# Kernel optimization log

Measured on AMD Instinct MI355X. Metric: run time of the kernel, lower is better.

## Reference

```python
import jax, jax.numpy as jnp
import numpy as np

K = 3
STRIDE = 1
PAD = 1


def _conv(x, w, b):
    # NCHW conv, OIHW weight, stride/pad fixed
    y = jax.lax.conv_general_dilated(
        x, w, (STRIDE, STRIDE), [(PAD, PAD), (PAD, PAD)],
        dimension_numbers=("NCHW", "OIHW", "NCHW"))
    if b is not None:
        y = y + b[None, :, None, None]
    return y


def _deform_conv2d(x, offset, mask, weight):
    """torchvision.ops.deform_conv2d (modulated, groups=1, dilation=1, no bias)."""
    B, C, H, W = x.shape
    O = weight.shape[0]
    KK = K * K
    Ho, Wo = offset.shape[2], offset.shape[3]
    off = offset.reshape(B, KK, 2, Ho, Wo)
    off_y, off_x = off[:, :, 0], off[:, :, 1]
    ky = (jnp.arange(KK) // K).astype(x.dtype)  # kernel row offset
    kx = (jnp.arange(KK) % K).astype(x.dtype)   # kernel col offset
    base_y = (jnp.arange(Ho) * STRIDE - PAD).astype(x.dtype)
    base_x = (jnp.arange(Wo) * STRIDE - PAD).astype(x.dtype)
    # sampling positions [B, KK, Ho, Wo]
    py = base_y[None, None, :, None] + ky[None, :, None, None] + off_y
    px = base_x[None, None, None, :] + kx[None, :, None, None] + off_x

    y0 = jnp.floor(py)
    x0 = jnp.floor(px)
    wy = py - y0  # fractional parts
    wx = px - x0

    x_flat = x.reshape(B, C, H * W)

    def gather(yy, xx):
        valid = (yy >= 0) & (yy < H) & (xx >= 0) & (xx < W)
        yc = jnp.clip(yy, 0, H - 1).astype(jnp.int32)
        xc = jnp.clip(xx, 0, W - 1).astype(jnp.int32)
        idx = (yc * W + xc).reshape(B, -1)  # [B, KK*Ho*Wo]
        v = jax.vmap(lambda a, i: a[:, i])(x_flat, idx)  # [B, C, KK*Ho*Wo]
        v = v.reshape(B, C, KK, Ho, Wo)
        return v * valid.astype(x.dtype).reshape(B, 1, KK, Ho, Wo)

    samp = (gather(y0, x0) * ((1 - wy) * (1 - wx))[:, None]
            + gather(y0, x0 + 1) * ((1 - wy) * wx)[:, None]
            + gather(y0 + 1, x0) * (wy * (1 - wx))[:, None]
            + gather(y0 + 1, x0 + 1) * (wy * wx)[:, None])
    samp = samp * mask[:, None]  # modulation [B, C, KK, Ho, Wo]
    return jnp.einsum('bckhw,ock->bohw', samp, weight.reshape(O, C, KK))


def setup_inputs() -> dict:
    key = jax.random.key(0)
    ks = jax.random.split(key, 6)
    B, Cin, H, W, Cout = 4, 128, 128, 128, 256
    KK = K * K
    x = jax.random.normal(ks[0], (B, Cin, H, W), dtype=jnp.float32)
    # offset conv: trained weights are small (init at 0) -> scale down
    offset_w = 0.01 * jax.random.normal(ks[1], (2 * KK, Cin, K, K), dtype=jnp.float32)
    offset_b = 0.1 * jax.random.normal(ks[2], (2 * KK,), dtype=jnp.float32)
    mod_w = 0.1 * jax.random.normal(ks[3], (KK, Cin, K, K), dtype=jnp.float32)
    mod_b = 0.1 * jax.random.normal(ks[4], (KK,), dtype=jnp.float32)
    fan_in = Cin * KK
    weight = jax.random.normal(ks[5], (Cout, Cin, K, K), dtype=jnp.float32) / np.sqrt(fan_in)
    return {"x": x, "offset_w": offset_w, "offset_b": offset_b,
            "mod_w": mod_w, "mod_b": mod_b, "weight": weight}


def reference(x, offset_w, offset_b, mod_w, mod_b, weight):
    offset = _conv(x, offset_w, offset_b)
    modulator = 2.0 * jax.nn.sigmoid(_conv(x, mod_w, mod_b))
    return _deform_conv2d(x, offset, modulator, weight)
```

## Files before the change

kernel.cpp:

```cpp
#include <hip/hip_runtime.h>
#include <hip/hip_bf16.h>
#include <math.h>

#define CIN 128
#define HH 128
#define WW 128
#define HWX (HH*WW)
#define COUT 256
#define NB 4

typedef __attribute__((ext_vector_type(8))) short short8;
typedef __attribute__((ext_vector_type(4))) float f32x4;
typedef __attribute__((ext_vector_type(8))) unsigned short ushort8;

__device__ __forceinline__ unsigned short f2bf(float f) {
    union { float f; unsigned int u; } c; c.f = f;
    unsigned int u = c.u + 0x7FFF + ((c.u >> 16) & 1);
    return (unsigned short)(u >> 16);
}

__global__ __launch_bounds__(256) void prep_kernel(
    const float* __restrict__ x, const float* __restrict__ wgt,
    const float* __restrict__ offw, const float* __restrict__ modw,
    float* __restrict__ xT, unsigned short* __restrict__ wAi,
    unsigned short* __restrict__ wCi)
{
    const int tid = threadIdx.x;
    const int bxg = blockIdx.x;

    if (bxg < 2048) {
        __shared__ float ls[32][132];
        const int bz = bxg;
        const int cg = bz & 3;
        const int y  = (bz >> 2) & 127;
        const int b  = bz >> 9;
        {
            int c  = tid >> 3;
            int x0 = (tid & 7) << 4;
            const float* src = x + (((size_t)(b * CIN + (cg << 5) + c)) << 14) + (y << 7) + x0;
#pragma unroll
            for (int k = 0; k < 4; ++k)
                *(f32x4*)&ls[c][x0 + 4 * k] = *(const f32x4*)(src + 4 * k);
        }
        __syncthreads();
        {
            int xc = tid >> 1;
            int h  = tid & 1;
            float v[16];
#pragma unroll
            for (int j = 0; j < 16; ++j) v[j] = ls[h * 16 + j][xc];
            float* dst = xT + ((((size_t)((b << 7) + y) << 7) + xc) << 7) + (cg << 5) + (h << 4);
#pragma unroll
            for (int k = 0; k < 4; ++k) {
                f32x4 t = { v[4 * k], v[4 * k + 1], v[4 * k + 2], v[4 * k + 3] };
                *(f32x4*)(dst + 4 * k) = t;
            }
        }
    } else if (bxg < 3200) {
        int i = (bxg - 2048) * 256 + tid;
        int j  = i & 7;
        int l  = (i >> 3) & 63;
        int mt = (i >> 9) & 15;
        int cc = (i >> 13) & 3;
        int kk = i >> 15;
        int o = mt * 16 + (l & 15);
        int c = cc * 32 + (l >> 4) * 8 + j;
        wAi[i] = f2bf(wgt[(o * CIN + c) * 9 + kk]);
    } else {
        int i = (bxg - 3200) * 256 + tid;
        if (i < 36864) {
            int j   = i & 7;
            int l   = (i >> 3) & 63;
            int mt  = (i >> 9) & 1;
            int q36 = i >> 10;
            int o = mt * 16 + (l & 15);
            int c = ((q36 & 3) << 5) + ((l >> 4) << 3) + j;
            int t = q36 >> 2;
            float v = 0.f;
            if (o < 18)      v = offw[(o * CIN + c) * 9 + t];
            else if (o < 27) v = modw[((o - 18) * CIN + c) * 9 + t];
            wCi[i] = f2bf(v);
        }
    }
}

__global__ __launch_bounds__(256) void convtab_kernel(
    const float* __restrict__ xT, const unsigned short* __restrict__ wCi,
    const float* __restrict__ offb, const float* __restrict__ modb,
    unsigned int* __restrict__ pk_out, float4* __restrict__ w4_out)
{
    __shared__ float outs[4][32][33];
    const int tid = threadIdx.x;
    const int wave = tid >> 6;
    const int l = tid & 63;
    const int bid = blockIdx.x;
    const int b = bid >> 7;
    const int y = bid & 127;
    const int x0 = wave << 5;
    const float* xb = xT + ((size_t)b << 21);

    f32x4 acc[2][2];
#pragma unroll
    for (int i = 0; i < 2; ++i)
#pragma unroll
        for (int j = 0; j < 2; ++j) acc[i][j] = (f32x4){0.f, 0.f, 0.f, 0.f};

    const int lp = l & 15;
    const int q8 = (l >> 4) << 3;

#pragma unroll 1
    for (int q36 = 0; q36 < 36; ++q36) {
        const int t  = q36 >> 2;
        const int c0 = (q36 & 3) << 5;
        const int ty = t / 3, tx = t - 3 * ty;
        const int yp = y + ty - 1;
        if (yp < 0 || yp >= HH) continue;

        const unsigned short* ap = wCi + (q36 << 10) + (l << 3);
        short8 af0 = *(const short8*)(ap);
        short8 af1 = *(const short8*)(ap + 512);

        short8 bf[2];
#pragma unroll
        for (int nt = 0; nt < 2; ++nt) {
            int xp = x0 + nt * 16 + lp + tx - 1;
            bool xin = (xp >= 0) && (xp < WW);
            const float* src = xb +
                ((((yp << 7) + (xin ? xp : 0)) << 7) + c0 + q8);
            f32x4 z = {0.f, 0.f, 0.f, 0.f};
            f32x4 lo = xin ? *(const f32x4*)src : z;
            f32x4 hi = xin ? *(const f32x4*)(src + 4) : z;
            union { unsigned int u[4]; short8 s8; } cv;
            asm("v_cvt_pk_bf16_f32 %0, %1, %2" : "=v"(cv.u[0]) : "v"(lo[0]), "v"(lo[1]));
            asm("v_cvt_pk_bf16_f32 %0, %1, %2" : "=v"(cv.u[1]) : "v"(lo[2]), "v"(lo[3]));
            asm("v_cvt_pk_bf16_f32 %0, %1, %2" : "=v"(cv.u[2]) : "v"(hi[0]), "v"(hi[1]));
            asm("v_cvt_pk_bf16_f32 %0, %1, %2" : "=v"(cv.u[3]) : "v"(hi[2]), "v"(hi[3]));
            bf[nt] = cv.s8;
        }
        acc[0][0] = __builtin_amdgcn_mfma_f32_16x16x32_bf16(af0, bf[0], acc[0][0], 0, 0, 0);
        acc[1][0] = __builtin_amdgcn_mfma_f32_16x16x32_bf16(af1, bf[0], acc[1][0], 0, 0, 0);
        acc[0][1] = __builtin_amdgcn_mfma_f32_16x16x32_bf16(af0, bf[1], acc[0][1], 0, 0, 0);
        acc[1][1] = __builtin_amdgcn_mfma_f32_16x16x32_bf16(af1, bf[1], acc[1][1], 0, 0, 0);
    }

    float (*po)[33] = outs[wave];
#pragma unroll
    for (int mt = 0; mt < 2; ++mt)
#pragma unroll
        for (int nt = 0; nt < 2; ++nt)
#pragma unroll
            for (int r = 0; r < 4; ++r)
                po[nt * 16 + lp][mt * 16 + (l >> 4) * 4 + r] = acc[mt][nt][r];

    const int pxe = l & 31;
    const int xw = x0 + pxe;
    const float* pe = &outs[wave][pxe][0];
#pragma unroll 1
    for (int kk = (l >> 5); kk < 9; kk += 2) {
        float oy = pe[2 * kk]     + offb[2 * kk];
        float ox = pe[2 * kk + 1] + offb[2 * kk + 1];
        float mt_ = pe[18 + kk]   + modb[kk];

        float m = 2.f / (1.f + expf(-mt_));
        float py = (float)(y - 1 + kk / 3) + oy;
        float px = (float)(xw - 1 + kk % 3) + ox;
        float y0f = floorf(py), x0f = floorf(px);
        float wy = py - y0f, wx = px - x0f;
        int y0 = (int)y0f, x0i = (int)x0f;
        int y1 = y0 + 1, x1 = x0i + 1;
        float vy0 = (y0 >= 0 && y0 < HH) ? 1.f : 0.f;
        float vy1 = (y1 >= 0 && y1 < HH) ? 1.f : 0.f;
        float vx0 = (x0i >= 0 && x0i < WW) ? 1.f : 0.f;
        float vx1 = (x1 >= 0 && x1 < WW) ? 1.f : 0.f;
        float a  = m * (1.f - wy) * vy0;
        float bb = m * wy * vy1;
        float u  = (1.f - wx) * vx0;
        float vv = wx * vx1;
        int y0c = min(max(y0, 0), HH - 1), y1c = min(max(y1, 0), HH - 1);
        int x0c = min(max(x0i, 0), WW - 1), x1c = min(max(x1, 0), WW - 1);
        int cb = min(max(x0i, 0), WW - 2);
        float wl = ((x0c == cb) ? u : 0.f) + ((x1c == cb) ? vv : 0.f);
        float wr = ((x0c == cb + 1) ? u : 0.f) + ((x1c == cb + 1) ? vv : 0.f);
        unsigned int pkv = (unsigned)y0c | ((unsigned)y1c << 7) |
                           ((unsigned)cb << 14);
        int gid = ((b * 9 + kk) << 14) + (y << 7) + xw;
        pk_out[gid] = pkv;
        w4_out[gid] = make_float4(a * wl, a * wr, bb * wl, bb * wr);
    }
}

__global__ __launch_bounds__(256, 2) void fused_kernel(
    const float* __restrict__ xT, const unsigned short* __restrict__ wAi,
    const unsigned int* __restrict__ pk, const float4* __restrict__ w4,
    float* __restrict__ out)
{
    __shared__ unsigned short Blds[2][4][4][512];
    __shared__ unsigned int tpk_l[576];
    __shared__ float4 tw_l[576];

    const int tid = threadIdx.x;
    const int wv = tid >> 6;
    const int l = tid & 63;
    const int bx = blockIdx.x;
    const int S = ((bx & 7) << 7) + (bx >> 3);
    const int lb = S >> 8;
    const int seg = S & 255;
    const int y = seg >> 1;
    const int x0 = (seg & 1) << 6;
    const float* xb = xT + ((size_t)lb << 21);
    const float colf = (l >= 32) ? 1.f : 0.f;
    unsigned char* BB = (unsigned char*)&Blds[0][0][0][0];

    {
        const int base = ((lb * 9) << 14) + (y << 7) + x0;
        for (int e = tid; e < 576; e += 256) {
            tpk_l[e] = pk[base + ((e >> 6) << 14) + (e & 63)];
            tw_l[e]  = w4[base + ((e >> 6) << 14) + (e & 63)];
        }
    }
    __syncthreads();

    f32x4 acc[4][4];
#pragma unroll
    for (int i = 0; i < 4; ++i)
#pragma unroll
        for (int j = 0; j < 4; ++j) acc[i][j] = (f32x4){0.f, 0.f, 0.f, 0.f};

#pragma unroll
    for (int st = 0; st < 4; ++st) {
        f32x4 r0[4], r1[4];
        float cw0[4], cw1[4];
#pragma unroll
        for (int p = 0; p < 4; ++p) {
            int e = (wv << 4) + (st << 2) + p;
            unsigned int pv = tpk_l[e];
            float4 twv = tw_l[e];
            cw0[p] = fmaf(twv.y - twv.x, colf, twv.x);
            cw1[p] = fmaf(twv.w - twv.z, colf, twv.z);
            const int y0c = pv & 127, y1c = (pv >> 7) & 127, cb = pv >> 14;
            r0[p] = *(const f32x4*)(xb + ((((y0c << 7) + cb) << 7) + (l << 2)));
            r1[p] = *(const f32x4*)(xb + ((((y1c << 7) + cb) << 7) + (l << 2)));
        }
#pragma unroll
        for (int p = 0; p < 4; ++p) {
            float res[4];
#pragma unroll
            for (int j = 0; j < 4; ++j) {
                float t = r0[p][j] * cw0[p] + r1[p][j] * cw1[p];
                res[j] = t + __shfl_xor(t, 32);
            }
            unsigned int d0, d1;
            asm("v_cvt_pk_bf16_f32 %0, %1, %2" : "=v"(d0) : "v"(res[0]), "v"(res[1]));
            asm("v_cvt_pk_bf16_f32 %0, %1, %2" : "=v"(d1) : "v"(res[2]), "v"(res[3]));
            if (l < 32) {
                int q  = (l >> 1) & 3;
                int h  = l & 1;
                int cw = l >> 3;
                int pxg = (st << 2) + p;
                int off = cw * 4096 + wv * 1024 +
                          (((q << 8) + (pxg << 4) + (h << 3)) ^
                           ((q << 5) ^ ((cw & 1) << 4)));
                uint2 dd; dd.x = d0; dd.y = d1;
                *(uint2*)(BB + off) = dd;
            }
        }
    }
    __syncthreads();

#pragma unroll 1
    for (int kk = 0; kk < 9; ++kk) {
        const int buf = kk & 1;
        const int nbo = (buf ^ 1) * 16384;
#pragma unroll
        for (int st = 0; st < 4; ++st) {
            const int cc = st;
            const unsigned short* ap =
                wAi + (((kk << 2) + cc) << 13) + (wv << 11) + (l << 3);
            short8 af[4];
#pragma unroll
            for (int mt = 0; mt < 4; ++mt)
                af[mt] = *(const short8*)(ap + (mt << 9));
            short8 bfr[4];
            {
                int ro = ((((l >> 4) << 8) + ((l & 15) << 4)) ^
                          (((l >> 4) << 5) ^ ((cc & 1) << 4)));
                const unsigned char* rb = BB + buf * 16384 + cc * 4096 + ro;
#pragma unroll
                for (int nt = 0; nt < 4; ++nt)
                    bfr[nt] = *(const short8*)(rb + nt * 1024);
            }
            f32x4 r0[4], r1[4];
            float cw0[4], cw1[4];
            if (kk < 8) {
#pragma unroll
                for (int p = 0; p < 4; ++p) {
                    int e = ((kk + 1) << 6) + (wv << 4) + (st << 2) + p;
                    unsigned int pv = tpk_l[e];
                    float4 twv = tw_l[e];
                    cw0[p] = fmaf(twv.y - twv.x, colf, twv.x);
                    cw1[p] = fmaf(twv.w - twv.z, colf, twv.z);
                    const int y0c = pv & 127, y1c = (pv >> 7) & 127, cb = pv >> 14;
                    r0[p] = *(const f32x4*)(xb + ((((y0c << 7) + cb) << 7) + (l << 2)));
                    r1[p] = *(const f32x4*)(xb + ((((y1c << 7) + cb) << 7) + (l << 2)));
                }
            }
            __builtin_amdgcn_s_setprio(1);
#pragma unroll
            for (int mt = 0; mt < 4; ++mt)
#pragma unroll
                for (int nt = 0; nt < 4; ++nt)
                    acc[mt][nt] = __builtin_amdgcn_mfma_f32_16x16x32_bf16(
                        af[mt], bfr[nt], acc[mt][nt], 0, 0, 0);
            __builtin_amdgcn_s_setprio(0);
            if (kk < 8) {
#pragma unroll
                for (int p = 0; p < 4; ++p) {
                    float res[4];
#pragma unroll
                    for (int j = 0; j < 4; ++j) {
                        float t = r0[p][j] * cw0[p] + r1[p][j] * cw1[p];
                        res[j] = t + __shfl_xor(t, 32);
                    }
                    unsigned int d0, d1;
                    asm("v_cvt_pk_bf16_f32 %0, %1, %2" : "=v"(d0) : "v"(res[0]), "v"(res[1]));
                    asm("v_cvt_pk_bf16_f32 %0, %1, %2" : "=v"(d1) : "v"(res[2]), "v"(res[3]));
                    if (l < 32) {
                        int q  = (l >> 1) & 3;
                        int h  = l & 1;
                        int cw = l >> 3;
                        int pxg = (st << 2) + p;
                        int off = nbo + cw * 4096 + wv * 1024 +
                                  (((q << 8) + (pxg << 4) + (h << 3)) ^
                                   ((q << 5) ^ ((cw & 1) << 4)));
                        uint2 dd; dd.x = d0; dd.y = d1;
                        *(uint2*)(BB + off) = dd;
                    }
                }
            }
        }
        __syncthreads();
    }

    const int crow = (l >> 4) * 4;
    const int pxl = (seg << 6) + (l & 15);
#pragma unroll
    for (int mt = 0; mt < 4; ++mt) {
#pragma unroll
        for (int nt = 0; nt < 4; ++nt) {
#pragma unroll
            for (int r = 0; r < 4; ++r) {
                int o = wv * 64 + mt * 16 + crow + r;
                out[(((size_t)(lb * COUT + o)) << 14) + pxl + nt * 16] =
                    acc[mt][nt][r];
            }
        }
    }
}

extern "C" void kernel_launch(void* const* d_in, const int* in_sizes, int n_in,
                              void* d_out, int out_size, void* d_ws, size_t ws_size,
                              hipStream_t stream)
{
    const float* x    = (const float*)d_in[0];
    const float* offw = (const float*)d_in[1];
    const float* offb = (const float*)d_in[2];
    const float* modw = (const float*)d_in[3];
    const float* modb = (const float*)d_in[4];
    const float* wgt  = (const float*)d_in[5];
    float* out = (float*)d_out;

    char* wsb = (char*)d_ws;
    unsigned int*   pkp = (unsigned int*)wsb;
    float4*         w4p = (float4*)(wsb + 2359296);
    unsigned short* wAi = (unsigned short*)(wsb + 11796480);
    unsigned short* wCi = (unsigned short*)(wsb + 12386304);
    float*          xTp = (float*)(wsb + 12460032);

    prep_kernel<<<dim3(3344), 256, 0, stream>>>(
        x, wgt, offw, modw, xTp, wAi, wCi);
    convtab_kernel<<<dim3(NB * HH), 256, 0, stream>>>(
        xTp, wCi, offb, modb, pkp, w4p);
    fused_kernel<<<dim3(NB * 256), 256, 0, stream>>>(
        xTp, wAi, pkp, w4p, out);
}
```

Baseline: 231.9 us.

## Halve fused kernel pixel tile to 32 and raise occupancy to five blocks

Shrinks each fused_kernel block from 64 to 32 output pixels, halving LDS tiles, per-wave accumulators and the table staging, and doubles the grid to 2048 blocks with launch_bounds raised to 5 waves per SIMD. The gather/bilinear pipeline is restructured so each kk step prefetches in one cc half and writes the next B tile in the other, spreading gather latency across the four MFMA chunks. The aim is more resident blocks and better latency hiding and CU fill. In exchange, every block reloads the full weight A tiles for half the pixels, doubling weight traffic per output, and the register cap may cause spills.

```diff
diff --git a/kernel.cpp b/kernel.cpp
--- a/kernel.cpp
+++ b/kernel.cpp
@@ -189,50 +189,50 @@
     }
 }
 
-__global__ __launch_bounds__(256, 2) void fused_kernel(
+__global__ __launch_bounds__(256, 5) void fused_kernel(
     const float* __restrict__ xT, const unsigned short* __restrict__ wAi,
     const unsigned int* __restrict__ pk, const float4* __restrict__ w4,
     float* __restrict__ out)
 {
-    __shared__ unsigned short Blds[2][4][4][512];
-    __shared__ unsigned int tpk_l[576];
-    __shared__ float4 tw_l[576];
+    __shared__ unsigned short Blds[2][4][2][512];
+    __shared__ unsigned int tpk_l[288];
+    __shared__ float4 tw_l[288];
 
     const int tid = threadIdx.x;
     const int wv = tid >> 6;
     const int l = tid & 63;
     const int bx = blockIdx.x;
-    const int S = ((bx & 7) << 7) + (bx >> 3);
-    const int lb = S >> 8;
-    const int seg = S & 255;
-    const int y = seg >> 1;
-    const int x0 = (seg & 1) << 6;
+    const int S = ((bx & 7) << 8) + (bx >> 3);
+    const int lb = S >> 9;
+    const int seg = S & 511;
+    const int y = seg >> 2;
+    const int x0 = (seg & 3) << 5;
     const float* xb = xT + ((size_t)lb << 21);
     const float colf = (l >= 32) ? 1.f : 0.f;
     unsigned char* BB = (unsigned char*)&Blds[0][0][0][0];
 
     {
         const int base = ((lb * 9) << 14) + (y << 7) + x0;
-        for (int e = tid; e < 576; e += 256) {
-            tpk_l[e] = pk[base + ((e >> 6) << 14) + (e & 63)];
-            tw_l[e]  = w4[base + ((e >> 6) << 14) + (e & 63)];
+        for (int e = tid; e < 288; e += 256) {
+            tpk_l[e] = pk[base + ((e >> 5) << 14) + (e & 31)];
+            tw_l[e]  = w4[base + ((e >> 5) << 14) + (e & 31)];
         }
     }
     __syncthreads();
 
-    f32x4 acc[4][4];
+    f32x4 acc[4][2];
 #pragma unroll
     for (int i = 0; i < 4; ++i)
 #pragma unroll
-        for (int j = 0; j < 4; ++j) acc[i][j] = (f32x4){0.f, 0.f, 0.f, 0.f};
-
-#pragma unroll
-    for (int st = 0; st < 4; ++st) {
+        for (int j = 0; j < 2; ++j) acc[i][j] = (f32x4){0.f, 0.f, 0.f, 0.f};
+
+#pragma unroll
+    for (int st = 0; st < 2; ++st) {
         f32x4 r0[4], r1[4];
         float cw0[4], cw1[4];
 #pragma unroll
         for (int p = 0; p < 4; ++p) {
-            int e = (wv << 4) + (st << 2) + p;
+            int e = (wv << 3) + (st << 2) + p;
             unsigned int pv = tpk_l[e];
             float4 twv = tw_l[e];
             cw0[p] = fmaf(twv.y - twv.x, colf, twv.x);
@@ -256,10 +256,10 @@
                 int q  = (l >> 1) & 3;
                 int h  = l & 1;
                 int cw = l >> 3;
-                int pxg = (st << 2) + p;
-                int off = cw * 4096 + wv * 1024 +
-                          (((q << 8) + (pxg << 4) + (h << 3)) ^
-                           ((q << 5) ^ ((cw & 1) << 4)));
+                int pxg = (wv << 3) + (st << 2) + p;
+                int off = cw * 2048 + (pxg >> 4) * 1024 +
+                          ((((q << 8) + ((pxg & 15) << 4) + (h << 3)) ^
+                            ((q << 5) ^ ((cw & 1) << 4))));
                 uint2 dd; dd.x = d0; dd.y = d1;
                 *(uint2*)(BB + off) = dd;
             }
@@ -270,55 +270,55 @@
 #pragma unroll 1
     for (int kk = 0; kk < 9; ++kk) {
         const int buf = kk & 1;
-        const int nbo = (buf ^ 1) * 16384;
-#pragma unroll
-        for (int st = 0; st < 4; ++st) {
-            const int cc = st;
+        const int nbo = (buf ^ 1) * 8192;
+        f32x4 pr0[4], pr1[4];
+        float pcw0[4], pcw1[4];
+#pragma unroll
+        for (int cc = 0; cc < 4; ++cc) {
             const unsigned short* ap =
                 wAi + (((kk << 2) + cc) << 13) + (wv << 11) + (l << 3);
             short8 af[4];
 #pragma unroll
             for (int mt = 0; mt < 4; ++mt)
                 af[mt] = *(const short8*)(ap + (mt << 9));
-            short8 bfr[4];
+            short8 bfr[2];
             {
                 int ro = ((((l >> 4) << 8) + ((l & 15) << 4)) ^
                           (((l >> 4) << 5) ^ ((cc & 1) << 4)));
-                const unsigned char* rb = BB + buf * 16384 + cc * 4096 + ro;
-#pragma unroll
-                for (int nt = 0; nt < 4; ++nt)
-                    bfr[nt] = *(const short8*)(rb + nt * 1024);
-            }
-            f32x4 r0[4], r1[4];
-            float cw0[4], cw1[4];
-            if (kk < 8) {
+                const unsigned char* rb = BB + buf * 8192 + cc * 2048 + ro;
+                bfr[0] = *(const short8*)(rb);
+                bfr[1] = *(const short8*)(rb + 1024);
+            }
+            if (kk < 8 && (cc & 1) == 0) {
+                const int st = cc >> 1;
 #pragma unroll
                 for (int p = 0; p < 4; ++p) {
-                    int e = ((kk + 1) << 6) + (wv << 4) + (st << 2) + p;
+                    int e = ((kk + 1) << 5) + (wv << 3) + (st << 2) + p;
                     unsigned int pv = tpk_l[e];
                     float4 twv = tw_l[e];
-                    cw0[p] = fmaf(twv.y - twv.x, colf, twv.x);
-                    cw1[p] = fmaf(twv.w - twv.z, colf, twv.z);
+                    pcw0[p] = fmaf(twv.y - twv.x, colf, twv.x);
+                    pcw1[p] = fmaf(twv.w - twv.z, colf, twv.z);
                     const int y0c = pv & 127, y1c = (pv >> 7) & 127, cb = pv >> 14;
-                    r0[p] = *(const f32x4*)(xb + ((((y0c << 7) + cb) << 7) + (l << 2)));
-                    r1[p] = *(const f32x4*)(xb + ((((y1c << 7) + cb) << 7) + (l << 2)));
+                    pr0[p] = *(const f32x4*)(xb + ((((y0c << 7) + cb) << 7) + (l << 2)));
+                    pr1[p] = *(const f32x4*)(xb + ((((y1c << 7) + cb) << 7) + (l << 2)));
                 }
             }
             __builtin_amdgcn_s_setprio(1);
 #pragma unroll
             for (int mt = 0; mt < 4; ++mt)
 #pragma unroll
-                for (int nt = 0; nt < 4; ++nt)
+                for (int nt = 0; nt < 2; ++nt)
                     acc[mt][nt] = __builtin_amdgcn_mfma_f32_16x16x32_bf16(
                         af[mt], bfr[nt], acc[mt][nt], 0, 0, 0);
             __builtin_amdgcn_s_setprio(0);
-            if (kk < 8) {
+            if (kk < 8 && (cc & 1) == 1) {
+                const int st = cc >> 1;
 #pragma unroll
                 for (int p = 0; p < 4; ++p) {
                     float res[4];
 #pragma unroll
                     for (int j = 0; j < 4; ++j) {
-                        float t = r0[p][j] * cw0[p] + r1[p][j] * cw1[p];
+                        float t = pr0[p][j] * pcw0[p] + pr1[p][j] * pcw1[p];
                         res[j] = t + __shfl_xor(t, 32);
                     }
                     unsigned int d0, d1;
@@ -328,10 +328,10 @@
                         int q  = (l >> 1) & 3;
                         int h  = l & 1;
                         int cw = l >> 3;
-                        int pxg = (st << 2) + p;
-                        int off = nbo + cw * 4096 + wv * 1024 +
-                                  (((q << 8) + (pxg << 4) + (h << 3)) ^
-                                   ((q << 5) ^ ((cw & 1) << 4)));
+                        int pxg = (wv << 3) + (st << 2) + p;
+                        int off = nbo + cw * 2048 + (pxg >> 4) * 1024 +
+                                  ((((q << 8) + ((pxg & 15) << 4) + (h << 3)) ^
+                                    ((q << 5) ^ ((cw & 1) << 4))));
                         uint2 dd; dd.x = d0; dd.y = d1;
                         *(uint2*)(BB + off) = dd;
                     }
@@ -342,15 +342,15 @@
     }
 
     const int crow = (l >> 4) * 4;
-    const int pxl = (seg << 6) + (l & 15);
 #pragma unroll
     for (int mt = 0; mt < 4; ++mt) {
 #pragma unroll
-        for (int nt = 0; nt < 4; ++nt) {
+        for (int nt = 0; nt < 2; ++nt) {
 #pragma unroll
             for (int r = 0; r < 4; ++r) {
-                int o = wv * 64 + mt * 16 + crow + r;
-                out[(((size_t)(lb * COUT + o)) << 14) + pxl + nt * 16] =
+                int o = (wv << 6) + mt * 16 + crow + r;
+                int pxl = (seg << 5) + nt * 16 + (l & 15);
+                out[(((size_t)(lb * COUT + o)) << 14) + pxl] =
                     acc[mt][nt][r];
             }
         }
@@ -380,6 +380,6 @@
         x, wgt, offw, modw, xTp, wAi, wCi);
     convtab_kernel<<<dim3(NB * HH), 256, 0, stream>>>(
         xTp, wCi, offb, modb, pkp, w4p);
-    fused_kernel<<<dim3(NB * 256), 256, 0, stream>>>(
+    fused_kernel<<<dim3(NB * 512), 256, 0, stream>>>(
         xTp, wAi, pkp, w4p, out);
 }
```

Result: slower. 535.6 us (+131.0%).

## Double-buffer weight fragments and defer gather combine by one stage

Applied to the files above, without the earlier changes.

The A-operand weight fragments for the next sub-step are now prefetched from global memory into a ping-pong register pair (afA/afB) before the current MFMA block, instead of being loaded just before use. The bilinear gather loads for stage cc are also issued one stage earlier, and their combine-and-store into the LDS B buffer is deferred to the following stage, with a tail flush after the loop. The goal is to hide global load latency behind MFMA work. In exchange the kernel holds more live vector registers, which could lower occupancy or cause spills.

```diff
diff --git a/kernel.cpp b/kernel.cpp
--- a/kernel.cpp
+++ b/kernel.cpp
@@ -265,21 +265,23 @@
             }
         }
     }
+    short8 afA[4], afB[4];
+    {
+        const unsigned short* ap = wAi + (wv << 11) + (l << 3);
+#pragma unroll
+        for (int mt = 0; mt < 4; ++mt)
+            afA[mt] = *(const short8*)(ap + (mt << 9));
+    }
     __syncthreads();
 
 #pragma unroll 1
     for (int kk = 0; kk < 9; ++kk) {
         const int buf = kk & 1;
         const int nbo = (buf ^ 1) * 16384;
-#pragma unroll
-        for (int st = 0; st < 4; ++st) {
-            const int cc = st;
-            const unsigned short* ap =
-                wAi + (((kk << 2) + cc) << 13) + (wv << 11) + (l << 3);
-            short8 af[4];
-#pragma unroll
-            for (int mt = 0; mt < 4; ++mt)
-                af[mt] = *(const short8*)(ap + (mt << 9));
+        f32x4 prA0[4], prA1[4], prB0[4], prB1[4];
+        float cwA0[4], cwA1[4], cwB0[4], cwB1[4];
+#pragma unroll
+        for (int cc = 0; cc < 4; ++cc) {
             short8 bfr[4];
             {
                 int ro = ((((l >> 4) << 8) + ((l & 15) << 4)) ^
@@ -289,36 +291,70 @@
                 for (int nt = 0; nt < 4; ++nt)
                     bfr[nt] = *(const short8*)(rb + nt * 1024);
             }
-            f32x4 r0[4], r1[4];
-            float cw0[4], cw1[4];
+            if (!(kk == 8 && cc == 3)) {
+                const int nkk = (cc < 3) ? kk : kk + 1;
+                const int ncc = (cc + 1) & 3;
+                const unsigned short* apn =
+                    wAi + (((nkk << 2) + ncc) << 13) + (wv << 11) + (l << 3);
+                if ((cc & 1) == 0) {
+#pragma unroll
+                    for (int mt = 0; mt < 4; ++mt)
+                        afB[mt] = *(const short8*)(apn + (mt << 9));
+                } else {
+#pragma unroll
+                    for (int mt = 0; mt < 4; ++mt)
+                        afA[mt] = *(const short8*)(apn + (mt << 9));
+                }
+            }
             if (kk < 8) {
 #pragma unroll
                 for (int p = 0; p < 4; ++p) {
-                    int e = ((kk + 1) << 6) + (wv << 4) + (st << 2) + p;
+                    int e = ((kk + 1) << 6) + (wv << 4) + (cc << 2) + p;
                     unsigned int pv = tpk_l[e];
                     float4 twv = tw_l[e];
-                    cw0[p] = fmaf(twv.y - twv.x, colf, twv.x);
-                    cw1[p] = fmaf(twv.w - twv.z, colf, twv.z);
                     const int y0c = pv & 127, y1c = (pv >> 7) & 127, cb = pv >> 14;
-                    r0[p] = *(const f32x4*)(xb + ((((y0c << 7) + cb) << 7) + (l << 2)));
-                    r1[p] = *(const f32x4*)(xb + ((((y1c << 7) + cb) << 7) + (l << 2)));
+                    const float* b0 = xb + ((((y0c << 7) + cb) << 7) + (l << 2));
+                    const float* b1 = xb + ((((y1c << 7) + cb) << 7) + (l << 2));
+                    if ((cc & 1) == 0) {
+                        cwA0[p] = fmaf(twv.y - twv.x, colf, twv.x);
+                        cwA1[p] = fmaf(twv.w - twv.z, colf, twv.z);
+                        prA0[p] = *(const f32x4*)b0;
+                        prA1[p] = *(const f32x4*)b1;
+                    } else {
+                        cwB0[p] = fmaf(twv.y - twv.x, colf, twv.x);
+                        cwB1[p] = fmaf(twv.w - twv.z, colf, twv.z);
+                        prB0[p] = *(const f32x4*)b0;
+                        prB1[p] = *(const f32x4*)b1;
+                    }
                 }
             }
             __builtin_amdgcn_s_setprio(1);
-#pragma unroll
-            for (int mt = 0; mt < 4; ++mt)
-#pragma unroll
-                for (int nt = 0; nt < 4; ++nt)
-                    acc[mt][nt] = __builtin_amdgcn_mfma_f32_16x16x32_bf16(
-                        af[mt], bfr[nt], acc[mt][nt], 0, 0, 0);
+            if ((cc & 1) == 0) {
+#pragma unroll
+                for (int mt = 0; mt < 4; ++mt)
+#pragma unroll
+                    for (int nt = 0; nt < 4; ++nt)
+                        acc[mt][nt] = __builtin_amdgcn_mfma_f32_16x16x32_bf16(
+                            afA[mt], bfr[nt], acc[mt][nt], 0, 0, 0);
+            } else {
+#pragma unroll
+                for (int mt = 0; mt < 4; ++mt)
+#pragma unroll
+                    for (int nt = 0; nt < 4; ++nt)
+                        acc[mt][nt] = __builtin_amdgcn_mfma_f32_16x16x32_bf16(
+                            afB[mt], bfr[nt], acc[mt][nt], 0, 0, 0);
+            }
             __builtin_amdgcn_s_setprio(0);
-            if (kk < 8) {
+            if (kk < 8 && cc >= 1) {
+                const int g = cc - 1;
 #pragma unroll
                 for (int p = 0; p < 4; ++p) {
                     float res[4];
 #pragma unroll
                     for (int j = 0; j < 4; ++j) {
-                        float t = r0[p][j] * cw0[p] + r1[p][j] * cw1[p];
+                        float t = ((g & 1) == 0)
+                            ? prA0[p][j] * cwA0[p] + prA1[p][j] * cwA1[p]
+                            : prB0[p][j] * cwB0[p] + prB1[p][j] * cwB1[p];
                         res[j] = t + __shfl_xor(t, 32);
                     }
                     unsigned int d0, d1;
@@ -328,13 +364,38 @@
                         int q  = (l >> 1) & 3;
                         int h  = l & 1;
                         int cw = l >> 3;
-                        int pxg = (st << 2) + p;
+                        int pxg = (g << 2) + p;
                         int off = nbo + cw * 4096 + wv * 1024 +
                                   (((q << 8) + (pxg << 4) + (h << 3)) ^
                                    ((q << 5) ^ ((cw & 1) << 4)));
                         uint2 dd; dd.x = d0; dd.y = d1;
                         *(uint2*)(BB + off) = dd;
                     }
+                }
+            }
+        }
+        if (kk < 8) {
+#pragma unroll
+            for (int p = 0; p < 4; ++p) {
+                float res[4];
+#pragma unroll
+                for (int j = 0; j < 4; ++j) {
+                    float t = prB0[p][j] * cwB0[p] + prB1[p][j] * cwB1[p];
+                    res[j] = t + __shfl_xor(t, 32);
+                }
+                unsigned int d0, d1;
+                asm("v_cvt_pk_bf16_f32 %0, %1, %2" : "=v"(d0) : "v"(res[0]), "v"(res[1]));
+                asm("v_cvt_pk_bf16_f32 %0, %1, %2" : "=v"(d1) : "v"(res[2]), "v"(res[3]));
+                if (l < 32) {
+                    int q  = (l >> 1) & 3;
+                    int h  = l & 1;
+                    int cw = l >> 3;
+                    int pxg = 12 + p;
+                    int off = nbo + cw * 4096 + wv * 1024 +
+                              (((q << 8) + (pxg << 4) + (h << 3)) ^
+                               ((q << 5) ^ ((cw & 1) << 4)));
+                    uint2 dd; dd.x = d0; dd.y = d1;
+                    *(uint2*)(BB + off) = dd;
                 }
             }
         }
```

Result: no change. 230.4 us (-0.6%).
